# Optimization experiments

Measured on AMD Instinct MI355X. Metric: run time of the kernel, lower is better.

Reference implementation:

```python
import jax, jax.numpy as jnp
import numpy as np

B, LQ, LK, D = 16, 2048, 2048, 256
NEG = -1e10


def setup_inputs() -> dict:
    key = jax.random.key(0)
    k1, k2, k3, k4, k5 = jax.random.split(key, 5)
    scale = 1.0 / np.sqrt(D)
    return {
        "x": jax.random.normal(k1, (B, LQ, D), dtype=jnp.float32),
        "y": jax.random.normal(k2, (B, LK, D), dtype=jnp.float32),
        "mask": jnp.zeros((B, LK), dtype=bool),  # True = padded key position
        "Wq": jax.random.normal(k3, (D, D), dtype=jnp.float32) * scale,
        "Wk": jax.random.normal(k4, (D, D), dtype=jnp.float32) * scale,
        "Wv": jax.random.normal(k5, (D, D), dtype=jnp.float32) * scale,
    }


def reference(x, y, mask, Wq, Wk, Wv):
    # nn.Linear: out = in @ W.T (no bias)
    q = jnp.einsum('bqd,ed->bqe', x, Wq)   # [B, LQ, D]
    k = jnp.einsum('bkd,ed->bke', y, Wk)   # [B, LK, D]
    v = jnp.einsum('bkd,ed->bke', y, Wv)   # [B, LK, D]
    # cdist (p=2) via GEMM expansion: ||q||^2 + ||k||^2 - 2 q.k
    qn = jnp.sum(q * q, axis=-1)                              # [B, LQ]
    kn = jnp.sum(k * k, axis=-1)                              # [B, LK]
    d2 = qn[:, :, None] + kn[:, None, :] - 2.0 * jnp.einsum('bqd,bkd->bqk', q, k)
    dist = jnp.sqrt(jnp.maximum(d2, 0.0))                     # [B, LQ, LK]
    scores = jnp.exp(-dist)
    # masked_fill: where original mask is True, set pre-softmax score to -1e10
    scores = jnp.where(mask[:, None, :], NEG, scores)
    attn = jax.nn.softmax(scores, axis=-1)                    # [B, LQ, LK]
    att_out = jnp.einsum('bqk,bkd->bqd', attn, v)             # [B, LQ, D]
    return (att_out, attn)
```

## Files before the change

kernel.cpp:

```cpp
#include <hip/hip_runtime.h>
#include <stdint.h>

#define B_   16
#define L_   2048
#define D_   256
#define NROW (B_*L_)

#define EPAD 40
#define TPAD 66

typedef __attribute__((ext_vector_type(8))) short s8v;
typedef __attribute__((ext_vector_type(4))) float f4v;
typedef __attribute__((ext_vector_type(4))) float f4n;

__device__ __forceinline__ unsigned short f2b(float f) {
    unsigned u = __builtin_bit_cast(unsigned, f);
    return (unsigned short)((u + 0x7fffu + ((u >> 16) & 1u)) >> 16);
}

__device__ __forceinline__ unsigned cvtpk(float a, float b) {
    unsigned r;
    asm("v_cvt_pk_bf16_f32 %0, %1, %2" : "=v"(r) : "v"(a), "v"(b));
    return r;
}

__device__ __forceinline__ void gl16(const void* g, void* l) {
    __builtin_amdgcn_global_load_lds(
        (const __attribute__((address_space(1))) unsigned int*)g,
        (__attribute__((address_space(3))) unsigned int*)l, 16, 0, 0);
}

template<int N> __device__ __forceinline__ void waitbar() {
    asm volatile("s_waitcnt vmcnt(%0)\n\ts_barrier" :: "i"(N) : "memory");
}
__device__ __forceinline__ void barOnly() {
    asm volatile("s_barrier" ::: "memory");
}

__global__ __launch_bounds__(256) void wconv_kernel(
    const float* __restrict__ Wq, const float* __restrict__ Wk,
    const float* __restrict__ Wv, unsigned short* __restrict__ Wb)
{
    const int t  = threadIdx.x;
    const int r0 = blockIdx.x * 64;
    const int wt = blockIdx.y;
    const float* W = wt == 0 ? Wq : (wt == 1 ? Wk : Wv);
    unsigned short* O = Wb + (size_t)wt * 256 * 256;
    #pragma unroll
    for (int p = 0; p < 16; ++p) {
        int idx  = p*256 + t;
        int row  = r0 + (idx >> 6);
        int half = idx & 1;
        int blk  = (idx & 63) >> 1;
        int c4   = blk*8 + half*4;
        float4 v = *(const float4*)(W + (size_t)row*D_ + c4);
        uint2 pw; pw.x = cvtpk(v.x, v.y); pw.y = cvtpk(v.z, v.w);
        *(uint2*)(O + row*256 + (blk ^ (row & 15))*8 + half*4) = pw;
    }
}

__device__ __forceinline__ void stage_W(const unsigned short* Wsrc, unsigned short* buf,
                                        int e0h, int w, int lane) {
    #pragma unroll
    for (int p = 0; p < 4; ++p) {
        int slot = p*256 + w*64 + lane;
        int row  = slot >> 5;
        int blk  = slot & 31;
        gl16(Wsrc + (size_t)(e0h + row)*256 + blk*8,
             buf + (size_t)(p*256 + w*64)*8);
    }
}

__global__ __launch_bounds__(256) void qkv_kernel(
    const float* __restrict__ x, const float* __restrict__ y,
    const unsigned short* __restrict__ Wb,
    unsigned short* __restrict__ Qb, unsigned short* __restrict__ Kb,
    unsigned short* __restrict__ Vt,
    float* __restrict__ qn, float* __restrict__ kn)
{
    __shared__ unsigned short Xs[64*256];
    __shared__ unsigned short Wsb[2][32*256];
    __shared__ unsigned short Ts[64*TPAD];

    const int t    = threadIdx.x;
    const int r0   = blockIdx.x * 64;
    const int type = blockIdx.y;
    const float* X = type ? y : x;

    #pragma unroll
    for (int p = 0; p < 16; ++p) {
        int idx  = p*256 + t;
        int row  = idx >> 6;
        int half = idx & 1;
        int blk  = (idx & 63) >> 1;
        int c4   = blk*8 + half*4;
        float4 vx = *(const float4*)(X + (size_t)(r0+row)*D_ + c4);
        uint2 px; px.x = cvtpk(vx.x, vx.y); px.y = cvtpk(vx.z, vx.w);
        *(uint2*)(Xs + row*256 + (blk ^ (row & 15))*8 + half*4) = px;
    }

    const int w = t >> 6, lane = t & 63, q16 = lane & 15, quad = lane >> 4;
    const int m0 = w * 16;

    const unsigned short* W0 = Wb + (type ? 65536 : 0);
    const unsigned short* W1 = Wb + 131072;

    stage_W(W0, Wsb[0], 0,  w, lane);
    stage_W(W0, Wsb[1], 32, w, lane);

    asm volatile("s_waitcnt vmcnt(4) lgkmcnt(0)\n\ts_barrier" ::: "memory");

    s8v xa[8];
    #pragma unroll
    for (int c = 0; c < 8; ++c)
        xa[c] = *(const s8v*)(Xs + (m0 + q16)*256 + (((c*4+quad) ^ q16)*8));

    float p4[4] = {0.f, 0.f, 0.f, 0.f};
    const f4v z4 = {0.f, 0.f, 0.f, 0.f};
    f4v acc[4];

    auto compute_half = [&](int par) {
        #pragma unroll
        for (int c = 0; c < 8; ++c)
            #pragma unroll
            for (int nn = 0; nn < 2; ++nn) {
                s8v bb = *(const s8v*)(Wsb[par] + (nn*16 + q16)*256 + (((c*4+quad) ^ q16)*8));
                acc[par*2+nn] = __builtin_amdgcn_mfma_f32_16x16x32_bf16(xa[c], bb, acc[par*2+nn], 0, 0, 0);
            }
    };

    auto epi_qk = [&](int ct) {
        unsigned short* Out = type ? Kb : Qb;
        #pragma unroll
        for (int n = 0; n < 4; ++n)
            #pragma unroll
            for (int r = 0; r < 4; ++r) {
                float v = acc[n][r];
                p4[r] += v * v;
                Out[(size_t)(r0 + m0 + quad*4 + r)*D_ + ct*64 + n*16 + q16] = f2b(v);
            }
    };

    auto epi_v = [&](int ct) {
        #pragma unroll
        for (int n = 0; n < 4; ++n)
            #pragma unroll
            for (int r = 0; r < 4; ++r)
                Ts[(m0 + quad*4 + r)*TPAD + n*16 + q16] = f2b(acc[n][r]);
        asm volatile("s_waitcnt lgkmcnt(0)\n\ts_barrier" ::: "memory");
        int j = t >> 2, kseg = t & 3;
        unsigned pk[8];
        #pragma unroll
        for (int i = 0; i < 8; ++i) {
            unsigned lo = Ts[(kseg*16 + 2*i    )*TPAD + j];
            unsigned hi = Ts[(kseg*16 + 2*i + 1)*TPAD + j];
            pk[i] = lo | (hi << 16);
        }
        int bb_ = r0 >> 11, k0g = r0 & (L_ - 1);
        unsigned short* dst = Vt + (size_t)(bb_*D_ + ct*64 + j)*L_ + k0g + kseg*16;
        *(uint4*)dst       = make_uint4(pk[0], pk[1], pk[2], pk[3]);
        *((uint4*)dst + 1) = make_uint4(pk[4], pk[5], pk[6], pk[7]);
    };

    if (!type) {
        #pragma unroll
        for (int h = 0; h < 8; ++h) {
            if (h == 7)      waitbar<0>();
            else if (h > 0) { if (h & 1) waitbar<4>(); else waitbar<20>(); }
            const int par = h & 1;
            acc[par*2] = z4; acc[par*2+1] = z4;
            compute_half(par);
            if (par) epi_qk(h >> 1);
            barOnly();
            if (h + 2 < 8) stage_W(W0, Wsb[par], (h+2)*32, w, lane);
        }
    } else {
        #pragma unroll
        for (int h = 0; h < 16; ++h) {
            if (h == 15)     waitbar<0>();
            else if (h > 0) {
                if (h & 1)       waitbar<4>();
                else if (h <= 8) waitbar<20>();
                else             waitbar<6>();
            }
            const int par = h & 1;
            acc[par*2] = z4; acc[par*2+1] = z4;
            compute_half(par);
            if (par) { if (h < 8) epi_qk(h >> 1); else epi_v((h - 8) >> 1); }
            barOnly();
            if (h + 2 < 16) {
                const unsigned short* Ws_ = (h + 2 < 8) ? W0 : W1;
                stage_W(Ws_, Wsb[par], ((h + 2) & 7) * 32, w, lane);
            }
        }
    }

    {
        float* norm = type ? kn : qn;
        #pragma unroll
        for (int r = 0; r < 4; ++r) {
            float v = p4[r];
            v += __shfl_xor(v, 1, 16);
            v += __shfl_xor(v, 2, 16);
            v += __shfl_xor(v, 4, 16);
            v += __shfl_xor(v, 8, 16);
            if (q16 == 0) norm[r0 + m0 + quad*4 + r] = v;
        }
    }
}

__device__ __forceinline__ void stage_K(const unsigned short* Kb, unsigned short* ks,
                                        int kb0, int k0, int w, int lane) {
    #pragma unroll
    for (int p = 0; p < 2; ++p) {
        int slot = p*512 + w*64 + lane;
        int row  = slot >> 5;
        int blk  = slot & 31;
        gl16(Kb + (size_t)(kb0 + k0 + row)*D_ + ((blk ^ (row & 15))*8),
             ks + (size_t)(p*512 + w*64)*8);
    }
}
__device__ __forceinline__ void stage_V(const unsigned short* Vt, unsigned short* vs,
                                        int bD, int kg0, int w, int lane) {
    #pragma unroll
    for (int p = 0; p < 2; ++p) {
        int slot = p*512 + w*64 + lane;
        int d    = slot >> 2;
        int blk  = slot & 3;
        gl16(Vt + (size_t)(bD + d)*L_ + kg0 + ((blk ^ ((d >> 1) & 3))*8),
             vs + (size_t)(p*512 + w*64)*8);
    }
}

__global__ __launch_bounds__(512, 2) void attnpv_kernel(
    const unsigned short* __restrict__ Qb, const unsigned short* __restrict__ Kb,
    const unsigned short* __restrict__ Vt,
    const float* __restrict__ qn, const float* __restrict__ kn,
    const unsigned char* __restrict__ mask,
    unsigned short* __restrict__ Eb,
    float* __restrict__ rs2, float* __restrict__ Op)
{
    __shared__ unsigned short Ks[3][32*256];
    __shared__ unsigned short Vs[3][256*32];
    __shared__ unsigned short Es[8][32*EPAD];
    __shared__ float         knS[1024];
    __shared__ unsigned int  mkS4[256];

    const int t  = threadIdx.x;
    const int s  = blockIdx.y * 16 + blockIdx.x;
    const int b  = ((s & 7) << 1) | (s >> 7);
    const int kh = (s >> 3) & 1;
    const int q0 = ((s >> 4) & 7) * 256;
    const int bk = b * L_;
    const int kb0 = bk + kh * 1024;
    const int bD = b * D_;
    const int w = t >> 6, lane = t & 63, q16 = lane & 15, quad = lane >> 4;
    const int qrow = bk + q0 + w*32;

    *(float2*)&knS[t*2] = *(const float2*)&kn[kb0 + t*2];
    if (t < 256) mkS4[t] = *(const unsigned int*)(mask + kb0 + t*4);

    s8v qa[2][8];
    float qnr[2][4];
    #pragma unroll
    for (int band = 0; band < 2; ++band) {
        #pragma unroll
        for (int c = 0; c < 8; ++c)
            qa[band][c] = *(const s8v*)(Qb + (size_t)(qrow + band*16 + q16)*D_ + c*32 + quad*8);
        #pragma unroll
        for (int r = 0; r < 4; ++r)
            qnr[band][r] = qn[qrow + band*16 + quad*4 + r];
    }

    unsigned short* ebase0 = Eb + (size_t)(qrow + (lane >> 2))*L_ + kh*1024 + (lane & 3)*8;
    unsigned short* ebase1 = ebase0 + (size_t)16*L_;
    const unsigned short* esrc0 = &Es[w][(lane >> 2)*EPAD + (lane & 3)*8];
    const unsigned short* esrc1 = esrc0 + 16*EPAD;

    float rs[2][4] = {{0.f,0.f,0.f,0.f},{0.f,0.f,0.f,0.f}};
    const f4v z4 = {0.f, 0.f, 0.f, 0.f};
    f4v O[2][16];
    #pragma unroll
    for (int band = 0; band < 2; ++band)
        #pragma unroll
        for (int n = 0; n < 16; ++n) O[band][n] = z4;

    auto do_tile = [&](int kt, const unsigned short* ksb, const unsigned short* vsb) {
        const int k0 = kt * 32;
        float kcv[2]; int mkv[2];
        #pragma unroll
        for (int n = 0; n < 2; ++n) {
            kcv[n] = knS[k0 + n*16 + q16];
            mkv[n] = ((const unsigned char*)mkS4)[k0 + n*16 + q16];
        }
        f4v S[2][2];
        S[0][0] = z4; S[0][1] = z4; S[1][0] = z4; S[1][1] = z4;
        __builtin_amdgcn_s_setprio(1);
        #pragma unroll
        for (int c = 0; c < 8; ++c)
            #pragma unroll
            for (int n = 0; n < 2; ++n) {
                s8v bb = *(const s8v*)(ksb + (n*16 + q16)*256 + (((c*4+quad) ^ q16)*8));
                S[0][n] = __builtin_amdgcn_mfma_f32_16x16x32_bf16(qa[0][c], bb, S[0][n], 0, 0, 0);
                S[1][n] = __builtin_amdgcn_mfma_f32_16x16x32_bf16(qa[1][c], bb, S[1][n], 0, 0, 0);
            }
        __builtin_amdgcn_s_setprio(0);
        #pragma unroll
        for (int band = 0; band < 2; ++band)
            #pragma unroll
            for (int n = 0; n < 2; ++n)
                #pragma unroll
                for (int r = 0; r < 4; ++r) {
                    float d2 = fmaf(-2.0f, S[band][n][r], qnr[band][r] + kcv[n]);
                    float dist = sqrtf(fmaxf(d2, 0.f));
                    float E = mkv[n] ? 0.f : __expf(__expf(-dist));
                    rs[band][r] += E;
                    Es[w][(band*16 + quad*4 + r)*EPAD + n*16 + q16] = f2b(E);
                }
        __builtin_nontemporal_store(*(const s8v*)esrc0, (s8v*)(ebase0 + k0));
        __builtin_nontemporal_store(*(const s8v*)esrc1, (s8v*)(ebase1 + k0));
        s8v af0 = *(const s8v*)(&Es[w][(q16     )*EPAD + quad*8]);
        s8v af1 = *(const s8v*)(&Es[w][(16 + q16)*EPAD + quad*8]);
        __builtin_amdgcn_s_setprio(1);
        #pragma unroll
        for (int n = 0; n < 16; ++n) {
            s8v vb = *(const s8v*)(vsb + (n*16 + q16)*32 +
                                   ((quad ^ ((q16 >> 1) & 3))*8));
            O[0][n] = __builtin_amdgcn_mfma_f32_16x16x32_bf16(af0, vb, O[0][n], 0, 0, 0);
            O[1][n] = __builtin_amdgcn_mfma_f32_16x16x32_bf16(af1, vb, O[1][n], 0, 0, 0);
        }
        __builtin_amdgcn_s_setprio(0);
    };

    stage_K(Kb, Ks[0], kb0, 0,  w, lane);  stage_V(Vt, Vs[0], bD, kh*1024 + 0,  w, lane);
    stage_K(Kb, Ks[1], kb0, 32, w, lane);  stage_V(Vt, Vs[1], bD, kh*1024 + 32, w, lane);
    asm volatile("s_waitcnt vmcnt(4) lgkmcnt(0)\n\ts_barrier" ::: "memory");
    stage_K(Kb, Ks[2], kb0, 64, w, lane);  stage_V(Vt, Vs[2], bD, kh*1024 + 64, w, lane);
    do_tile(0, Ks[0], Vs[0]);

    for (int kt = 1; kt < 31; ++kt) {
        if (kt == 1) { asm volatile("s_waitcnt vmcnt(6)\n\ts_barrier" ::: "memory"); }
        else         { asm volatile("s_waitcnt vmcnt(8)\n\ts_barrier" ::: "memory"); }
        if (kt < 30) {
            int nb = kt + 2; nb -= (nb >= 3) ? 3 : 0; nb -= (nb >= 3) ? 3 : 0;
            nb = (kt + 2) % 3;
            stage_K(Kb, Ks[nb], kb0, (kt+2)*32, w, lane);
            stage_V(Vt, Vs[nb], bD, kh*1024 + (kt+2)*32, w, lane);
        }
        do_tile(kt, Ks[kt % 3], Vs[kt % 3]);
    }
    asm volatile("s_waitcnt vmcnt(4)\n\ts_barrier" ::: "memory");
    do_tile(31, Ks[31 % 3], Vs[31 % 3]);

    #pragma unroll
    for (int band = 0; band < 2; ++band) {
        #pragma unroll
        for (int r = 0; r < 4; ++r) {
            float v = rs[band][r];
            v += __shfl_xor(v, 1, 16);
            v += __shfl_xor(v, 2, 16);
            v += __shfl_xor(v, 4, 16);
            v += __shfl_xor(v, 8, 16);
            if (q16 == 0) rs2[(size_t)kh*NROW + qrow + band*16 + quad*4 + r] = v;
        }
        #pragma unroll
        for (int n = 0; n < 16; ++n)
            #pragma unroll
            for (int r = 0; r < 4; ++r)
                __builtin_nontemporal_store(O[band][n][r],
                    Op + (size_t)kh*NROW*D_ +
                        (size_t)(qrow + band*16 + quad*4 + r)*D_ + n*16 + q16);
    }
}

__global__ __launch_bounds__(256) void norm_kernel(
    const unsigned short* __restrict__ Eb,
    const float* __restrict__ rs2, const float* __restrict__ Op,
    float* __restrict__ att_out, float* __restrict__ attn_out)
{
    const int row = blockIdx.x;
    const int t   = threadIdx.x;
    const float inv = 1.0f / (rs2[row] + rs2[NROW + row]);
    const size_t base = (size_t)row * L_ + t*8;

    s8v e = __builtin_nontemporal_load((const s8v*)(Eb + base));
    f4n o0, o1;
    o0.x = __builtin_bit_cast(float, ((unsigned)(unsigned short)e[0]) << 16) * inv;
    o0.y = __builtin_bit_cast(float, ((unsigned)(unsigned short)e[1]) << 16) * inv;
    o0.z = __builtin_bit_cast(float, ((unsigned)(unsigned short)e[2]) << 16) * inv;
    o0.w = __builtin_bit_cast(float, ((unsigned)(unsigned short)e[3]) << 16) * inv;
    o1.x = __builtin_bit_cast(float, ((unsigned)(unsigned short)e[4]) << 16) * inv;
    o1.y = __builtin_bit_cast(float, ((unsigned)(unsigned short)e[5]) << 16) * inv;
    o1.z = __builtin_bit_cast(float, ((unsigned)(unsigned short)e[6]) << 16) * inv;
    o1.w = __builtin_bit_cast(float, ((unsigned)(unsigned short)e[7]) << 16) * inv;
    __builtin_nontemporal_store(o0, (f4n*)(attn_out + base));
    __builtin_nontemporal_store(o1, (f4n*)(attn_out + base + 4));

    if (t < 32) {
        const size_t ob = (size_t)row * D_ + t*8;
        f4n a0 = *(const f4n*)(Op + ob);
        f4n a1 = *(const f4n*)(Op + ob + 4);
        f4n b0 = *(const f4n*)(Op + (size_t)NROW*D_ + ob);
        f4n b1 = *(const f4n*)(Op + (size_t)NROW*D_ + ob + 4);
        f4n r0_ = (a0 + b0) * inv;
        f4n r1_ = (a1 + b1) * inv;
        __builtin_nontemporal_store(r0_, (f4n*)(att_out + ob));
        __builtin_nontemporal_store(r1_, (f4n*)(att_out + ob + 4));
    }
}

extern "C" void kernel_launch(void* const* d_in, const int* in_sizes, int n_in,
                              void* d_out, int out_size, void* d_ws, size_t ws_size,
                              hipStream_t stream) {
    (void)in_sizes; (void)n_in; (void)out_size; (void)ws_size;
    const float* x  = (const float*)d_in[0];
    const float* y  = (const float*)d_in[1];
    const unsigned char* mask = (const unsigned char*)d_in[2];
    const float* Wq = (const float*)d_in[3];
    const float* Wk = (const float*)d_in[4];
    const float* Wv = (const float*)d_in[5];

    char* ws = (char*)d_ws;
    unsigned short* Qb = (unsigned short*)ws;
    unsigned short* Kb = Qb + (size_t)NROW * D_;
    unsigned short* Vt = Kb + (size_t)NROW * D_;
    float* qn  = (float*)(ws + 3 * (size_t)NROW * D_ * 2);
    float* kn  = qn + NROW;
    float* rs2 = kn + NROW;
    unsigned short* Eb = (unsigned short*)(rs2 + 2*(size_t)NROW);
    float* Op = (float*)(Eb + (size_t)NROW * L_);
    unsigned short* Wb = (unsigned short*)(Op + 2*(size_t)NROW*D_);

    float* att_out = (float*)d_out;
    float* attn    = att_out + (size_t)NROW * D_;

    wconv_kernel<<<dim3(4, 3), 256, 0, stream>>>(Wq, Wk, Wv, Wb);
    qkv_kernel<<<dim3(512, 2), 256, 0, stream>>>(x, y, Wb, Qb, Kb, Vt, qn, kn);
    attnpv_kernel<<<dim3(16, 16), 512, 0, stream>>>(Qb, Kb, Vt, qn, kn, mask,
                                                    Eb, rs2, Op);
    norm_kernel<<<dim3(NROW), 256, 0, stream>>>(Eb, rs2, Op, att_out, attn);
}
```

Baseline: 594.5 us.

## Halve per-wave query rows, use double buffering, raise attention kernel occupancy

Each wave of the attention kernel now handles 16 query rows instead of 32. K/V staging drops from a triple to a double buffer, the grid doubles to 512 blocks and launch bounds ask for 4 blocks per CU. The aim is to cut registers and LDS per block so more waves run at once and hide latency. In exchange each K/V tile loaded into LDS feeds only half as many query rows, which doubles K/V traffic from global memory. The shallower prefetch pipeline, waiting with vmcnt(1) before every tile, also exposes more load latency.

```diff
diff --git a/kernel.cpp b/kernel.cpp
--- a/kernel.cpp
+++ b/kernel.cpp
@@ -232,7 +232,7 @@
     }
 }
 
-__global__ __launch_bounds__(512, 2) void attnpv_kernel(
+__global__ __launch_bounds__(512, 4) void attnpv_kernel(
     const unsigned short* __restrict__ Qb, const unsigned short* __restrict__ Kb,
     const unsigned short* __restrict__ Vt,
     const float* __restrict__ qn, const float* __restrict__ kn,
@@ -240,50 +240,43 @@
     unsigned short* __restrict__ Eb,
     float* __restrict__ rs2, float* __restrict__ Op)
 {
-    __shared__ unsigned short Ks[3][32*256];
-    __shared__ unsigned short Vs[3][256*32];
-    __shared__ unsigned short Es[8][32*EPAD];
+    __shared__ unsigned short Ks[2][32*256];
+    __shared__ unsigned short Vs[2][256*32];
+    __shared__ unsigned short Es[8][16*EPAD];
     __shared__ float         knS[1024];
     __shared__ unsigned int  mkS4[256];
 
     const int t  = threadIdx.x;
-    const int s  = blockIdx.y * 16 + blockIdx.x;
-    const int b  = ((s & 7) << 1) | (s >> 7);
-    const int kh = (s >> 3) & 1;
-    const int q0 = ((s >> 4) & 7) * 256;
+    const int s  = blockIdx.y * 32 + blockIdx.x;
+    const int b  = ((s & 7) << 1) | (s >> 8);
+    const int kh = (s >> 7) & 1;
+    const int q0 = ((s >> 3) & 15) * 128;
     const int bk = b * L_;
     const int kb0 = bk + kh * 1024;
     const int bD = b * D_;
     const int w = t >> 6, lane = t & 63, q16 = lane & 15, quad = lane >> 4;
-    const int qrow = bk + q0 + w*32;
+    const int qrow = bk + q0 + w*16;
 
     *(float2*)&knS[t*2] = *(const float2*)&kn[kb0 + t*2];
     if (t < 256) mkS4[t] = *(const unsigned int*)(mask + kb0 + t*4);
 
-    s8v qa[2][8];
-    float qnr[2][4];
-    #pragma unroll
-    for (int band = 0; band < 2; ++band) {
-        #pragma unroll
-        for (int c = 0; c < 8; ++c)
-            qa[band][c] = *(const s8v*)(Qb + (size_t)(qrow + band*16 + q16)*D_ + c*32 + quad*8);
-        #pragma unroll
-        for (int r = 0; r < 4; ++r)
-            qnr[band][r] = qn[qrow + band*16 + quad*4 + r];
-    }
-
-    unsigned short* ebase0 = Eb + (size_t)(qrow + (lane >> 2))*L_ + kh*1024 + (lane & 3)*8;
-    unsigned short* ebase1 = ebase0 + (size_t)16*L_;
-    const unsigned short* esrc0 = &Es[w][(lane >> 2)*EPAD + (lane & 3)*8];
-    const unsigned short* esrc1 = esrc0 + 16*EPAD;
-
-    float rs[2][4] = {{0.f,0.f,0.f,0.f},{0.f,0.f,0.f,0.f}};
+    s8v qa[8];
+    float qnr[4];
+    #pragma unroll
+    for (int c = 0; c < 8; ++c)
+        qa[c] = *(const s8v*)(Qb + (size_t)(qrow + q16)*D_ + c*32 + quad*8);
+    #pragma unroll
+    for (int r = 0; r < 4; ++r)
+        qnr[r] = qn[qrow + quad*4 + r];
+
+    unsigned short* ebase = Eb + (size_t)(qrow + (lane >> 2))*L_ + kh*1024 + (lane & 3)*8;
+    const unsigned short* esrc = &Es[w][(lane >> 2)*EPAD + (lane & 3)*8];
+
+    float rs[4] = {0.f, 0.f, 0.f, 0.f};
     const f4v z4 = {0.f, 0.f, 0.f, 0.f};
-    f4v O[2][16];
-    #pragma unroll
-    for (int band = 0; band < 2; ++band)
-        #pragma unroll
-        for (int n = 0; n < 16; ++n) O[band][n] = z4;
+    f4v O[16];
+    #pragma unroll
+    for (int n = 0; n < 16; ++n) O[n] = z4;
 
     auto do_tile = [&](int kt, const unsigned short* ksb, const unsigned short* vsb) {
         const int k0 = kt * 32;
@@ -293,41 +286,33 @@
             kcv[n] = knS[k0 + n*16 + q16];
             mkv[n] = ((const unsigned char*)mkS4)[k0 + n*16 + q16];
         }
-        f4v S[2][2];
-        S[0][0] = z4; S[0][1] = z4; S[1][0] = z4; S[1][1] = z4;
-        __builtin_amdgcn_s_setprio(1);
-        #pragma unroll
-        for (int c = 0; c < 8; ++c)
+        #pragma unroll
+        for (int n = 0; n < 2; ++n) {
+            f4v s4 = z4;
+            __builtin_amdgcn_s_setprio(1);
             #pragma unroll
-            for (int n = 0; n < 2; ++n) {
+            for (int c = 0; c < 8; ++c) {
                 s8v bb = *(const s8v*)(ksb + (n*16 + q16)*256 + (((c*4+quad) ^ q16)*8));
-                S[0][n] = __builtin_amdgcn_mfma_f32_16x16x32_bf16(qa[0][c], bb, S[0][n], 0, 0, 0);
-                S[1][n] = __builtin_amdgcn_mfma_f32_16x16x32_bf16(qa[1][c], bb, S[1][n], 0, 0, 0);
-            }
-        __builtin_amdgcn_s_setprio(0);
-        #pragma unroll
-        for (int band = 0; band < 2; ++band)
+                s4 = __builtin_amdgcn_mfma_f32_16x16x32_bf16(qa[c], bb, s4, 0, 0, 0);
+            }
+            __builtin_amdgcn_s_setprio(0);
             #pragma unroll
-            for (int n = 0; n < 2; ++n)
-                #pragma unroll
-                for (int r = 0; r < 4; ++r) {
-                    float d2 = fmaf(-2.0f, S[band][n][r], qnr[band][r] + kcv[n]);
-                    float dist = sqrtf(fmaxf(d2, 0.f));
-                    float E = mkv[n] ? 0.f : __expf(__expf(-dist));
-                    rs[band][r] += E;
-                    Es[w][(band*16 + quad*4 + r)*EPAD + n*16 + q16] = f2b(E);
-                }
-        __builtin_nontemporal_store(*(const s8v*)esrc0, (s8v*)(ebase0 + k0));
-        __builtin_nontemporal_store(*(const s8v*)esrc1, (s8v*)(ebase1 + k0));
-        s8v af0 = *(const s8v*)(&Es[w][(q16     )*EPAD + quad*8]);
-        s8v af1 = *(const s8v*)(&Es[w][(16 + q16)*EPAD + quad*8]);
+            for (int r = 0; r < 4; ++r) {
+                float d2 = fmaf(-2.0f, s4[r], qnr[r] + kcv[n]);
+                float dist = sqrtf(fmaxf(d2, 0.f));
+                float E = mkv[n] ? 0.f : __expf(__expf(-dist));
+                rs[r] += E;
+                Es[w][(quad*4 + r)*EPAD + n*16 + q16] = f2b(E);
+            }
+        }
+        __builtin_nontemporal_store(*(const s8v*)esrc, (s8v*)(ebase + k0));
+        s8v af = *(const s8v*)(&Es[w][q16*EPAD + quad*8]);
         __builtin_amdgcn_s_setprio(1);
         #pragma unroll
         for (int n = 0; n < 16; ++n) {
             s8v vb = *(const s8v*)(vsb + (n*16 + q16)*32 +
                                    ((quad ^ ((q16 >> 1) & 3))*8));
-            O[0][n] = __builtin_amdgcn_mfma_f32_16x16x32_bf16(af0, vb, O[0][n], 0, 0, 0);
-            O[1][n] = __builtin_amdgcn_mfma_f32_16x16x32_bf16(af1, vb, O[1][n], 0, 0, 0);
+            O[n] = __builtin_amdgcn_mfma_f32_16x16x32_bf16(af, vb, O[n], 0, 0, 0);
         }
         __builtin_amdgcn_s_setprio(0);
     };
@@ -335,42 +320,34 @@
     stage_K(Kb, Ks[0], kb0, 0,  w, lane);  stage_V(Vt, Vs[0], bD, kh*1024 + 0,  w, lane);
     stage_K(Kb, Ks[1], kb0, 32, w, lane);  stage_V(Vt, Vs[1], bD, kh*1024 + 32, w, lane);
     asm volatile("s_waitcnt vmcnt(4) lgkmcnt(0)\n\ts_barrier" ::: "memory");
-    stage_K(Kb, Ks[2], kb0, 64, w, lane);  stage_V(Vt, Vs[2], bD, kh*1024 + 64, w, lane);
     do_tile(0, Ks[0], Vs[0]);
 
-    for (int kt = 1; kt < 31; ++kt) {
-        if (kt == 1) { asm volatile("s_waitcnt vmcnt(6)\n\ts_barrier" ::: "memory"); }
-        else         { asm volatile("s_waitcnt vmcnt(8)\n\ts_barrier" ::: "memory"); }
-        if (kt < 30) {
-            int nb = kt + 2; nb -= (nb >= 3) ? 3 : 0; nb -= (nb >= 3) ? 3 : 0;
-            nb = (kt + 2) % 3;
-            stage_K(Kb, Ks[nb], kb0, (kt+2)*32, w, lane);
-            stage_V(Vt, Vs[nb], bD, kh*1024 + (kt+2)*32, w, lane);
-        }
-        do_tile(kt, Ks[kt % 3], Vs[kt % 3]);
-    }
-    asm volatile("s_waitcnt vmcnt(4)\n\ts_barrier" ::: "memory");
-    do_tile(31, Ks[31 % 3], Vs[31 % 3]);
-
-    #pragma unroll
-    for (int band = 0; band < 2; ++band) {
-        #pragma unroll
-        for (int r = 0; r < 4; ++r) {
-            float v = rs[band][r];
-            v += __shfl_xor(v, 1, 16);
-            v += __shfl_xor(v, 2, 16);
-            v += __shfl_xor(v, 4, 16);
-            v += __shfl_xor(v, 8, 16);
-            if (q16 == 0) rs2[(size_t)kh*NROW + qrow + band*16 + quad*4 + r] = v;
-        }
-        #pragma unroll
-        for (int n = 0; n < 16; ++n)
-            #pragma unroll
-            for (int r = 0; r < 4; ++r)
-                __builtin_nontemporal_store(O[band][n][r],
-                    Op + (size_t)kh*NROW*D_ +
-                        (size_t)(qrow + band*16 + quad*4 + r)*D_ + n*16 + q16);
-    }
+    for (int kt = 1; kt < 32; ++kt) {
+        asm volatile("s_waitcnt vmcnt(1)\n\ts_barrier" ::: "memory");
+        if (kt < 31) {
+            const int nb = (kt + 1) & 1;
+            stage_K(Kb, Ks[nb], kb0, (kt+1)*32, w, lane);
+            stage_V(Vt, Vs[nb], bD, kh*1024 + (kt+1)*32, w, lane);
+        }
+        do_tile(kt, Ks[kt & 1], Vs[kt & 1]);
+    }
+
+    #pragma unroll
+    for (int r = 0; r < 4; ++r) {
+        float v = rs[r];
+        v += __shfl_xor(v, 1, 16);
+        v += __shfl_xor(v, 2, 16);
+        v += __shfl_xor(v, 4, 16);
+        v += __shfl_xor(v, 8, 16);
+        if (q16 == 0) rs2[(size_t)kh*NROW + qrow + quad*4 + r] = v;
+    }
+    #pragma unroll
+    for (int n = 0; n < 16; ++n)
+        #pragma unroll
+        for (int r = 0; r < 4; ++r)
+            __builtin_nontemporal_store(O[n][r],
+                Op + (size_t)kh*NROW*D_ +
+                    (size_t)(qrow + quad*4 + r)*D_ + n*16 + q16);
 }
 
 __global__ __launch_bounds__(256) void norm_kernel(
@@ -436,7 +413,7 @@
 
     wconv_kernel<<<dim3(4, 3), 256, 0, stream>>>(Wq, Wk, Wv, Wb);
     qkv_kernel<<<dim3(512, 2), 256, 0, stream>>>(x, y, Wb, Qb, Kb, Vt, qn, kn);
-    attnpv_kernel<<<dim3(16, 16), 512, 0, stream>>>(Qb, Kb, Vt, qn, kn, mask,
+    attnpv_kernel<<<dim3(32, 16), 512, 0, stream>>>(Qb, Kb, Vt, qn, kn, mask,
                                                     Eb, rs2, Op);
     norm_kernel<<<dim3(NROW), 256, 0, stream>>>(Eb, rs2, Op, att_out, attn);
 }
```

After: 704.4 us. +18.5%, slower.
